# Kernel tuning notes

Hardware: AMD Instinct MI355X
Metric: run time of the kernel (lower is better)

Reference implementation:

```python
import jax, jax.numpy as jnp
import numpy as np

B, L, D, H, NL = 4, 2048, 1024, 4, 2
HD = D // H
FF = 4 * D
EPS = 1e-5


def layernorm(x, g, b):
    mu = jnp.mean(x, axis=-1, keepdims=True)
    var = jnp.mean(jnp.square(x - mu), axis=-1, keepdims=True)
    return (x - mu) * jax.lax.rsqrt(var + EPS) * g + b


def setup_inputs() -> dict:
    key = jax.random.key(0)
    ks = jax.random.split(key, 8)
    std = 0.02
    return {
        "x": jax.random.normal(ks[0], (B, L, 3 * D), dtype=jnp.float32),
        "w3d": jax.random.normal(ks[1], (D, 3 * D), dtype=jnp.float32) * std,
        "b3d": jnp.zeros((D,), jnp.float32),
        "ln1_g": jnp.ones((NL, D), jnp.float32),
        "ln1_b": jnp.zeros((NL, D), jnp.float32),
        "wqkv": jax.random.normal(ks[2], (NL, 3 * D, D), dtype=jnp.float32) * std,
        "bqkv": jnp.zeros((NL, 3 * D), jnp.float32),
        "wproj": jax.random.normal(ks[3], (NL, D, D), dtype=jnp.float32) * std,
        "bproj": jnp.zeros((NL, D), jnp.float32),
        "ln2_g": jnp.ones((NL, D), jnp.float32),
        "ln2_b": jnp.zeros((NL, D), jnp.float32),
        "w1": jax.random.normal(ks[4], (NL, FF, D), dtype=jnp.float32) * std,
        "b1": jnp.zeros((NL, FF), jnp.float32),
        "w2": jax.random.normal(ks[5], (NL, D, FF), dtype=jnp.float32) * std,
        "b2": jnp.zeros((NL, D), jnp.float32),
        "lnf_g": jnp.ones((D,), jnp.float32),
        "lnf_b": jnp.zeros((D,), jnp.float32),
    }


def reference(x, w3d, b3d, ln1_g, ln1_b, wqkv, bqkv, wproj, bproj,
              ln2_g, ln2_b, w1, b1, w2, b2, lnf_g, lnf_b):
    h = jnp.einsum('bli,di->bld', x, w3d) + b3d
    scale = 1.0 / jnp.sqrt(jnp.float32(HD))
    for i in range(NL):
        # attention block
        res = h
        hn = layernorm(h, ln1_g[i], ln1_b[i])
        qkv = jnp.einsum('bld,ed->ble', hn, wqkv[i]) + bqkv[i]  # [B,L,3D]
        qkv = qkv.reshape(B, L, 3, H, HD)
        q, k, v = qkv[:, :, 0], qkv[:, :, 1], qkv[:, :, 2]  # [B,L,H,HD]
        attn = jnp.einsum('bqhd,bkhd->bhqk', q, k) * scale
        attn = jax.nn.softmax(attn, axis=-1)
        o = jnp.einsum('bhqk,bkhd->bqhd', attn, v).reshape(B, L, D)
        h = res + jnp.einsum('bld,ed->ble', o, wproj[i]) + bproj[i]
        # FFN block
        res = h
        hn = layernorm(h, ln2_g[i], ln2_b[i])
        f = jnp.einsum('bld,fd->blf', hn, w1[i]) + b1[i]
        f = jax.nn.gelu(f, approximate=False)  # torch nn.GELU default is exact
        h = res + jnp.einsum('blf,df->bld', f, w2[i]) + b2[i]
    return layernorm(h, lnf_g, lnf_b)
```

## Files before the change

### kernel.cpp

```cpp
#include <hip/hip_runtime.h>
#include <cstdint>
#include <cstddef>

#define BATCH   4
#define L_SEQ   2048
#define DMODEL  1024
#define NHEAD   4
#define HDIM    256
#define FFDIM   4096
#define MROWS   (BATCH * L_SEQ)
#define NLAYER  2

typedef __bf16 bf16_t;
typedef __bf16 bf16x8 __attribute__((ext_vector_type(8)));
typedef __bf16 bf16x4 __attribute__((ext_vector_type(4)));
typedef float  floatx4 __attribute__((ext_vector_type(4)));

__device__ __forceinline__ void async_cp16(const void* g, void* l) {
  auto gp = reinterpret_cast<__attribute__((address_space(1))) void*>(
      reinterpret_cast<uintptr_t>(g));
  auto lp = reinterpret_cast<__attribute__((address_space(3))) void*>(
      reinterpret_cast<uintptr_t>(l));
  __builtin_amdgcn_global_load_lds(gp, lp, 16, 0, 0);
}

__global__ __launch_bounds__(256)
void cvt_f32_bf16(const float* __restrict__ in, bf16_t* __restrict__ out, int n4) {
  int i = blockIdx.x * 256 + threadIdx.x;
  if (i >= n4) return;
  float4 v = ((const float4*)in)[i];
  bf16x4 ov = { (bf16_t)v.x, (bf16_t)v.y, (bf16_t)v.z, (bf16_t)v.w };
  ((bf16x4*)out)[i] = ov;
}

template<bool BF16OUT>
__global__ __launch_bounds__(256)
void ln_kernel(const float* __restrict__ x, const float* __restrict__ gw,
               const float* __restrict__ bw, void* __restrict__ outp) {
  const int row = blockIdx.x;
  const int tid = threadIdx.x;
  const float4 v = ((const float4*)(x + (size_t)row * DMODEL))[tid];
  float s  = v.x + v.y + v.z + v.w;
  float ss = v.x * v.x + v.y * v.y + v.z * v.z + v.w * v.w;
#pragma unroll
  for (int o = 32; o > 0; o >>= 1) {
    s  += __shfl_xor(s, o);
    ss += __shfl_xor(ss, o);
  }
  __shared__ float red0[4], red1[4];
  const int wv = tid >> 6;
  if ((tid & 63) == 0) { red0[wv] = s; red1[wv] = ss; }
  __syncthreads();
  s  = red0[0] + red0[1] + red0[2] + red0[3];
  ss = red1[0] + red1[1] + red1[2] + red1[3];
  const float mu  = s * (1.0f / DMODEL);
  const float var = ss * (1.0f / DMODEL) - mu * mu;
  const float rs  = rsqrtf(var + 1e-5f);
  const float4 g4 = ((const float4*)gw)[tid];
  const float4 b4 = ((const float4*)bw)[tid];
  const float o0 = (v.x - mu) * rs * g4.x + b4.x;
  const float o1 = (v.y - mu) * rs * g4.y + b4.y;
  const float o2 = (v.z - mu) * rs * g4.z + b4.z;
  const float o3 = (v.w - mu) * rs * g4.w + b4.w;
  if (BF16OUT) {
    bf16x4 ov = { (bf16_t)o0, (bf16_t)o1, (bf16_t)o2, (bf16_t)o3 };
    ((bf16x4*)outp)[(size_t)row * (DMODEL / 4) + tid] = ov;
  } else {
    float4 ov = { o0, o1, o2, o3 };
    ((float4*)outp)[(size_t)row * (DMODEL / 4) + tid] = ov;
  }
}

__global__ __launch_bounds__(256)
void softmax_kernel(bf16_t* __restrict__ S) {
  const size_t row = blockIdx.x;
  bf16_t* p = S + row * (size_t)L_SEQ + (size_t)threadIdx.x * 8;
  bf16x8 rv = *(const bf16x8*)p;
  float v[8];
  float mx = -1e30f;
#pragma unroll
  for (int j = 0; j < 8; ++j) { v[j] = (float)rv[j]; mx = fmaxf(mx, v[j]); }
#pragma unroll
  for (int o = 32; o > 0; o >>= 1) mx = fmaxf(mx, __shfl_xor(mx, o));
  __shared__ float sm[4], ssum[4];
  const int lane = threadIdx.x & 63, wv = threadIdx.x >> 6;
  if (lane == 0) sm[wv] = mx;
  __syncthreads();
  mx = fmaxf(fmaxf(sm[0], sm[1]), fmaxf(sm[2], sm[3]));
  float sum = 0.0f;
#pragma unroll
  for (int j = 0; j < 8; ++j) { v[j] = __expf(v[j] - mx); sum += v[j]; }
#pragma unroll
  for (int o = 32; o > 0; o >>= 1) sum += __shfl_xor(sum, o);
  if (lane == 0) ssum[wv] = sum;
  __syncthreads();
  sum = ssum[0] + ssum[1] + ssum[2] + ssum[3];
  const float inv = 1.0f / sum;
  bf16x8 ov;
#pragma unroll
  for (int j = 0; j < 8; ++j) ov[j] = (bf16_t)(v[j] * inv);
  *(bf16x8*)p = ov;
}

__global__ __launch_bounds__(256)
void transpose_v(const bf16_t* __restrict__ vt, bf16_t* __restrict__ vT) {
  __shared__ bf16_t tile[64][65];
  const int z = blockIdx.z, b = z >> 2, head = z & 3;
  const int l0 = blockIdx.x * 64, hd0 = blockIdx.y * 64;
  const int x = threadIdx.x & 63, y4 = threadIdx.x >> 6;
#pragma unroll
  for (int r = 0; r < 64; r += 4) {
    const int l = l0 + y4 + r;
    tile[y4 + r][x] =
        vt[((size_t)b * L_SEQ + l) * DMODEL + head * HDIM + hd0 + x];
  }
  __syncthreads();
#pragma unroll
  for (int r = 0; r < 64; r += 4) {
    const int hd = hd0 + y4 + r;
    vT[((size_t)z * HDIM + hd) * L_SEQ + l0 + x] = tile[x][y4 + r];
  }
}

struct EpiBiasF32 {
  float* C; const float* bias; int ldc;
  __device__ __forceinline__ void store(int, int m, int n, float v) const {
    C[(size_t)m * ldc + n] = v + bias[n];
  }
};
struct EpiResBiasF32 {
  float* C; const float* bias; int ldc;
  __device__ __forceinline__ void store(int, int m, int n, float v) const {
    const size_t idx = (size_t)m * ldc + n;
    C[idx] = C[idx] + v + bias[n];
  }
};
struct EpiGeluBf16 {
  bf16_t* C; const float* bias; int ldc;
  __device__ __forceinline__ void store(int, int m, int n, float v) const {
    const float t = v + bias[n];
    const float g = 0.5f * t * (1.0f + erff(t * 0.7071067811865475f));
    C[(size_t)m * ldc + n] = (bf16_t)g;
  }
};
struct EpiQKV {
  bf16_t *q, *k, *vt; const float* bias;
  __device__ __forceinline__ void store(int, int m, int n, float v) const {
    const float t = v + bias[n];
    const int b = m >> 11, l = m & 2047;
    const int which = n >> 10, e = n & 1023;
    const int head = e >> 8, hd = e & 255;
    const bf16_t x = (bf16_t)t;
    if (which == 0)
      q[(((size_t)(b * NHEAD + head)) * L_SEQ + l) * HDIM + hd] = x;
    else if (which == 1)
      k[(((size_t)(b * NHEAD + head)) * L_SEQ + l) * HDIM + hd] = x;
    else
      vt[(size_t)m * DMODEL + e] = x;
  }
};
struct EpiScaleBf16 {
  bf16_t* C; long strideC; int ldc; float scale;
  __device__ __forceinline__ void store(int z, int m, int n, float v) const {
    C[(size_t)z * strideC + (size_t)m * ldc + n] = (bf16_t)(v * scale);
  }
};
struct EpiOBf16 {
  bf16_t* C;
  __device__ __forceinline__ void store(int z, int m, int n, float v) const {
    C[((size_t)(z >> 2) * L_SEQ + m) * DMODEL + (z & 3) * HDIM + n] = (bf16_t)v;
  }
};

template<class Epi>
__global__ __launch_bounds__(256, 2)
void gemm_bt(const bf16_t* __restrict__ A, int lda, long strideA,
             const bf16_t* __restrict__ B, int ldb, long strideB,
             int K, Epi epi) {
  __shared__ bf16_t lsA[128 * 32];
  __shared__ bf16_t lsB[128 * 32];
  const int tid  = threadIdx.x;
  const int wave = tid >> 6, lane = tid & 63;
  const int z = blockIdx.z;
  A += (size_t)z * strideA;
  B += (size_t)z * strideB;
  const int m0 = blockIdx.y * 128, n0 = blockIdx.x * 128;

  const int c   = (lane & 3) * 8;
  const int r0  = (wave * 2 + 0) * 16 + (lane >> 2);
  const int r1  = (wave * 2 + 1) * 16 + (lane >> 2);
  const bf16_t* ga0 = A + (size_t)(m0 + r0) * lda + c;
  const bf16_t* ga1 = A + (size_t)(m0 + r1) * lda + c;
  const bf16_t* gb0 = B + (size_t)(n0 + r0) * ldb + c;
  const bf16_t* gb1 = B + (size_t)(n0 + r1) * ldb + c;
  bf16_t* la0 = &lsA[(wave * 2 + 0) * 512];
  bf16_t* la1 = &lsA[(wave * 2 + 1) * 512];
  bf16_t* lb0 = &lsB[(wave * 2 + 0) * 512];
  bf16_t* lb1 = &lsB[(wave * 2 + 1) * 512];

  const int wm = wave >> 1, wn = wave & 1;
  const int lane15 = lane & 15, quad = lane >> 4;
  const int aoff = (wm * 64 + lane15) * 32 + quad * 8;
  const int boff = (wn * 64 + lane15) * 32 + quad * 8;

  floatx4 acc[4][4] = {};

  for (int k0 = 0; k0 < K; k0 += 32) {
    async_cp16(ga0 + k0, la0);
    async_cp16(ga1 + k0, la1);
    async_cp16(gb0 + k0, lb0);
    async_cp16(gb1 + k0, lb1);
    __syncthreads();
    bf16x8 af[4], bfr[4];
#pragma unroll
    for (int i = 0; i < 4; ++i) af[i]  = *(const bf16x8*)&lsA[aoff + i * 512];
#pragma unroll
    for (int i = 0; i < 4; ++i) bfr[i] = *(const bf16x8*)&lsB[boff + i * 512];
#pragma unroll
    for (int i = 0; i < 4; ++i)
#pragma unroll
      for (int j = 0; j < 4; ++j)
        acc[i][j] = __builtin_amdgcn_mfma_f32_16x16x32_bf16(af[i], bfr[j],
                                                            acc[i][j], 0, 0, 0);
    __syncthreads();
  }

#pragma unroll
  for (int i = 0; i < 4; ++i) {
    const int mbase = m0 + wm * 64 + i * 16 + quad * 4;
#pragma unroll
    for (int j = 0; j < 4; ++j) {
      const int nloc = n0 + wn * 64 + j * 16 + lane15;
#pragma unroll
      for (int r = 0; r < 4; ++r)
        epi.store(z, mbase + r, nloc, acc[i][j][r]);
    }
  }
}

extern "C" void kernel_launch(void* const* d_in, const int* in_sizes, int n_in,
                              void* d_out, int out_size, void* d_ws, size_t ws_size,
                              hipStream_t stream) {
  const float* x_in  = (const float*)d_in[0];
  const float* w3d   = (const float*)d_in[1];
  const float* b3d   = (const float*)d_in[2];
  const float* ln1g  = (const float*)d_in[3];
  const float* ln1b  = (const float*)d_in[4];
  const float* wqkv  = (const float*)d_in[5];
  const float* bqkv  = (const float*)d_in[6];
  const float* wproj = (const float*)d_in[7];
  const float* bproj = (const float*)d_in[8];
  const float* ln2g  = (const float*)d_in[9];
  const float* ln2b  = (const float*)d_in[10];
  const float* w1    = (const float*)d_in[11];
  const float* b1    = (const float*)d_in[12];
  const float* w2    = (const float*)d_in[13];
  const float* b2    = (const float*)d_in[14];
  const float* lnfg  = (const float*)d_in[15];
  const float* lnfb  = (const float*)d_in[16];
  float* out = (float*)d_out;

  char* ws = (char*)d_ws;
  size_t off = 0;
  auto alloc = [&](size_t bytes) -> void* {
    void* p = ws + off;
    off = (off + bytes + 255) & ~(size_t)255;
    return p;
  };
  float*  h      = (float*) alloc((size_t)MROWS * DMODEL * 4);
  bf16_t* hn     = (bf16_t*)alloc((size_t)MROWS * DMODEL * 2);
  bf16_t* w3db   = (bf16_t*)alloc((size_t)DMODEL * 3 * DMODEL * 2);
  bf16_t* wqkvb  = (bf16_t*)alloc((size_t)NLAYER * 3 * DMODEL * DMODEL * 2);
  bf16_t* wprojb = (bf16_t*)alloc((size_t)NLAYER * DMODEL * DMODEL * 2);
  bf16_t* w1b    = (bf16_t*)alloc((size_t)NLAYER * FFDIM * DMODEL * 2);
  bf16_t* w2b    = (bf16_t*)alloc((size_t)NLAYER * DMODEL * FFDIM * 2);
  char*   r1     = (char*)  alloc(3ull * 16777216);
  bf16_t* xb     = (bf16_t*)r1;
  bf16_t* qb     = (bf16_t*)r1;
  bf16_t* kb     = (bf16_t*)(r1 + 16777216);
  bf16_t* vtmp   = (bf16_t*)(r1 + 2ull * 16777216);
  bf16_t* vT     = (bf16_t*)alloc(16777216);
  bf16_t* ob     = (bf16_t*)alloc(16777216);
  char*   r2     = (char*)  alloc(134217728);
  bf16_t* S      = (bf16_t*)r2;
  bf16_t* f      = (bf16_t*)r2;
  (void)ws_size; (void)in_sizes; (void)n_in; (void)out_size;

  auto cvt = [&](const float* src, bf16_t* dst, size_t n) {
    int n4 = (int)(n / 4);
    cvt_f32_bf16<<<(n4 + 255) / 256, 256, 0, stream>>>(src, dst, n4);
  };
  cvt(x_in,  xb,     (size_t)MROWS * 3 * DMODEL);
  cvt(w3d,   w3db,   (size_t)DMODEL * 3 * DMODEL);
  cvt(wqkv,  wqkvb,  (size_t)NLAYER * 3 * DMODEL * DMODEL);
  cvt(wproj, wprojb, (size_t)NLAYER * DMODEL * DMODEL);
  cvt(w1,    w1b,    (size_t)NLAYER * FFDIM * DMODEL);
  cvt(w2,    w2b,    (size_t)NLAYER * DMODEL * FFDIM);

  gemm_bt<<<dim3(DMODEL / 128, MROWS / 128, 1), 256, 0, stream>>>(
      xb, 3 * DMODEL, 0L, w3db, 3 * DMODEL, 0L, 3 * DMODEL,
      EpiBiasF32{h, b3d, DMODEL});

  for (int i = 0; i < NLAYER; ++i) {
    ln_kernel<true><<<MROWS, 256, 0, stream>>>(h, ln1g + i * DMODEL,
                                               ln1b + i * DMODEL, hn);
    gemm_bt<<<dim3(3 * DMODEL / 128, MROWS / 128, 1), 256, 0, stream>>>(
        hn, DMODEL, 0L, wqkvb + (size_t)i * 3 * DMODEL * DMODEL, DMODEL, 0L,
        DMODEL, EpiQKV{qb, kb, vtmp, bqkv + i * 3 * DMODEL});
    transpose_v<<<dim3(L_SEQ / 64, HDIM / 64, BATCH * NHEAD), 256, 0, stream>>>(
        vtmp, vT);
    gemm_bt<<<dim3(L_SEQ / 128, L_SEQ / 128, BATCH * NHEAD), 256, 0, stream>>>(
        qb, HDIM, (long)L_SEQ * HDIM, kb, HDIM, (long)L_SEQ * HDIM, HDIM,
        EpiScaleBf16{S, (long)L_SEQ * L_SEQ, L_SEQ, 0.0625f});
    softmax_kernel<<<BATCH * NHEAD * L_SEQ, 256, 0, stream>>>(S);
    gemm_bt<<<dim3(HDIM / 128, L_SEQ / 128, BATCH * NHEAD), 256, 0, stream>>>(
        S, L_SEQ, (long)L_SEQ * L_SEQ, vT, L_SEQ, (long)HDIM * L_SEQ, L_SEQ,
        EpiOBf16{ob});
    gemm_bt<<<dim3(DMODEL / 128, MROWS / 128, 1), 256, 0, stream>>>(
        ob, DMODEL, 0L, wprojb + (size_t)i * DMODEL * DMODEL, DMODEL, 0L,
        DMODEL, EpiResBiasF32{h, bproj + i * DMODEL, DMODEL});
    ln_kernel<true><<<MROWS, 256, 0, stream>>>(h, ln2g + i * DMODEL,
                                               ln2b + i * DMODEL, hn);
    gemm_bt<<<dim3(FFDIM / 128, MROWS / 128, 1), 256, 0, stream>>>(
        hn, DMODEL, 0L, w1b + (size_t)i * FFDIM * DMODEL, DMODEL, 0L, DMODEL,
        EpiGeluBf16{f, b1 + i * FFDIM, FFDIM});
    gemm_bt<<<dim3(DMODEL / 128, MROWS / 128, 1), 256, 0, stream>>>(
        f, FFDIM, 0L, w2b + (size_t)i * DMODEL * FFDIM, FFDIM, 0L, FFDIM,
        EpiResBiasF32{h, b2 + i * DMODEL, DMODEL});
  }

  ln_kernel<false><<<MROWS, 256, 0, stream>>>(h, lnfg, lnfb, out);
}
```

Baseline: 1.462 ms.

## Double GEMM K-tile to 64 with XOR-swizzled LDS layout

Raises the GEMM K step from 32 to 64 per barrier pair, halving the number of sync points. It stores A/B tiles in LDS with an XOR swizzle on the 16-byte column chunk so the MFMA fragment reads avoid bank conflicts. Launch bounds are raised to 3 blocks per CU. LDS use doubles to 32KB per block, and the tighter register bound may cause spills.

```diff
diff --git a/kernel.cpp b/kernel.cpp
--- a/kernel.cpp
+++ b/kernel.cpp
@@ -173,12 +173,12 @@
 };
 
 template<class Epi>
-__global__ __launch_bounds__(256, 2)
+__global__ __launch_bounds__(256, 3)
 void gemm_bt(const bf16_t* __restrict__ A, int lda, long strideA,
              const bf16_t* __restrict__ B, int ldb, long strideB,
              int K, Epi epi) {
-  __shared__ bf16_t lsA[128 * 32];
-  __shared__ bf16_t lsB[128 * 32];
+  __shared__ bf16_t lsA[128 * 64];
+  __shared__ bf16_t lsB[128 * 64];
   const int tid  = threadIdx.x;
   const int wave = tid >> 6, lane = tid & 63;
   const int z = blockIdx.z;
@@ -186,42 +186,48 @@
   B += (size_t)z * strideB;
   const int m0 = blockIdx.y * 128, n0 = blockIdx.x * 128;
 
-  const int c   = (lane & 3) * 8;
-  const int r0  = (wave * 2 + 0) * 16 + (lane >> 2);
-  const int r1  = (wave * 2 + 1) * 16 + (lane >> 2);
-  const bf16_t* ga0 = A + (size_t)(m0 + r0) * lda + c;
-  const bf16_t* ga1 = A + (size_t)(m0 + r1) * lda + c;
-  const bf16_t* gb0 = B + (size_t)(n0 + r0) * ldb + c;
-  const bf16_t* gb1 = B + (size_t)(n0 + r1) * ldb + c;
-  bf16_t* la0 = &lsA[(wave * 2 + 0) * 512];
-  bf16_t* la1 = &lsA[(wave * 2 + 1) * 512];
-  bf16_t* lb0 = &lsB[(wave * 2 + 0) * 512];
-  bf16_t* lb1 = &lsB[(wave * 2 + 1) * 512];
+  const int rl = lane >> 3, p = lane & 7;
+  const int csw = (p ^ rl) * 8;
+  const int rbase = wave * 32 + rl;
+  const bf16_t* gA = A + (size_t)(m0 + rbase) * lda + csw;
+  const bf16_t* gB = B + (size_t)(n0 + rbase) * ldb + csw;
+  bf16_t* lA = &lsA[wave * 32 * 64];
+  bf16_t* lB = &lsB[wave * 32 * 64];
 
   const int wm = wave >> 1, wn = wave & 1;
   const int lane15 = lane & 15, quad = lane >> 4;
-  const int aoff = (wm * 64 + lane15) * 32 + quad * 8;
-  const int boff = (wn * 64 + lane15) * 32 + quad * 8;
+  const int arow = wm * 64 + lane15;
+  const int brow = wn * 64 + lane15;
+  const int sw = lane15 & 7;
+  const int koff0 = ((quad + 0) ^ sw) * 8;
+  const int koff1 = ((quad + 4) ^ sw) * 8;
 
   floatx4 acc[4][4] = {};
 
-  for (int k0 = 0; k0 < K; k0 += 32) {
-    async_cp16(ga0 + k0, la0);
-    async_cp16(ga1 + k0, la1);
-    async_cp16(gb0 + k0, lb0);
-    async_cp16(gb1 + k0, lb1);
+  for (int k0 = 0; k0 < K; k0 += 64) {
+#pragma unroll
+    for (int j = 0; j < 4; ++j) {
+      async_cp16(gA + k0 + (size_t)j * 8 * lda, lA + j * 8 * 64);
+      async_cp16(gB + k0 + (size_t)j * 8 * ldb, lB + j * 8 * 64);
+    }
     __syncthreads();
-    bf16x8 af[4], bfr[4];
-#pragma unroll
-    for (int i = 0; i < 4; ++i) af[i]  = *(const bf16x8*)&lsA[aoff + i * 512];
-#pragma unroll
-    for (int i = 0; i < 4; ++i) bfr[i] = *(const bf16x8*)&lsB[boff + i * 512];
-#pragma unroll
-    for (int i = 0; i < 4; ++i)
+#pragma unroll
+    for (int kk = 0; kk < 2; ++kk) {
+      const int ko = kk ? koff1 : koff0;
+      bf16x8 af[4], bfr[4];
+#pragma unroll
+      for (int i = 0; i < 4; ++i)
+        af[i] = *(const bf16x8*)&lsA[(arow + i * 16) * 64 + ko];
 #pragma unroll
       for (int j = 0; j < 4; ++j)
-        acc[i][j] = __builtin_amdgcn_mfma_f32_16x16x32_bf16(af[i], bfr[j],
-                                                            acc[i][j], 0, 0, 0);
+        bfr[j] = *(const bf16x8*)&lsB[(brow + j * 16) * 64 + ko];
+#pragma unroll
+      for (int i = 0; i < 4; ++i)
+#pragma unroll
+        for (int j = 0; j < 4; ++j)
+          acc[i][j] = __builtin_amdgcn_mfma_f32_16x16x32_bf16(af[i], bfr[j],
+                                                              acc[i][j], 0, 0, 0);
+    }
     __syncthreads();
   }
 
```

Result: faster. 1.323 ms (-9.5%).
